# Performance work log

Measured on AMD Instinct MI355X. Metric: run time of the kernel, lower is better.

## Reference

```python
import jax, jax.numpy as jnp
import numpy as np

PATCH = 16      # sqrt(n_patches=256)
ALPHA = 10.0
HEADS, DH = 2, 64


def _fourier(coords, Bm):
    # coords: (HW, 2), Bm: (n_features, 2) -> (HW, 2*n_features)
    proj = 2.0 * jnp.pi * coords @ Bm.T
    return jnp.concatenate([jnp.cos(proj), jnp.sin(proj)], axis=-1)


def _forward(coords_decoding, tokens, B_q, B_l0, B_l1,
             qW, qb, toqW, tokvW, tooW, toob,
             bwW0, bwb0, bwW1, bwb1,
             modW0, modb0, modW1, modb1,
             hvW0, hvb0, outW0, outb0, outW1, outb1):
    B = coords_decoding.shape[0]
    Hh, Ww = coords_decoding.shape[1], coords_decoding.shape[2]
    coords = coords_decoding.reshape(B, -1, coords_decoding.shape[-1])
    grid = coords[0]                      # (HW, 2); coords_modulation is None -> same grid
    HW = grid.shape[0]
    m = tokens.shape[1]

    # patch indices and spatial bias
    row = jnp.clip((grid[:, 0] * PATCH).astype(jnp.int32), 0, PATCH - 1)
    col = jnp.clip((grid[:, 1] * PATCH).astype(jnp.int32), 0, PATCH - 1)
    idx = row * PATCH + col               # (HW,)
    t = idx.astype(jnp.float32) / (PATCH * PATCH)
    pos = (jnp.arange(m, dtype=jnp.float32) + 0.5) / m
    rel = -ALPHA * jnp.abs(t[None, :] - pos[:, None]) ** 2   # (m, HW)
    bias = rel.T                          # (HW, m), broadcast over batch & heads

    # query features (shared across batch)
    xq = jax.nn.relu(_fourier(grid, B_q) @ qW + qb)           # (HW, hd)
    xq_b = jnp.broadcast_to(xq[None], (B, HW, xq.shape[-1]))

    # cross attention with spatial bias
    q = (xq_b @ toqW).reshape(B, HW, HEADS, DH).transpose(0, 2, 1, 3)   # (B,h,HW,Dh)
    kv = tokens @ tokvW                                                  # (B,m,2*inner)
    k, v = jnp.split(kv, 2, axis=-1)
    k = k.reshape(B, m, HEADS, DH).transpose(0, 2, 1, 3)                 # (B,h,m,Dh)
    v = v.reshape(B, m, HEADS, DH).transpose(0, 2, 1, 3)
    sim = jnp.einsum('bhqd,bhkd->bhqk', q, k) * (DH ** -0.5) + bias[None, None]
    attn = jax.nn.softmax(sim, axis=-1)
    o = jnp.einsum('bhqk,bhkd->bhqd', attn, v)
    o = o.transpose(0, 2, 1, 3).reshape(B, HW, HEADS * DH)
    mod = o @ tooW + toob                                                # (B,HW,hd)

    # per-band MLP stack (layer_num = 2)
    def band(Bl, bwW, bwb, mW, mb):
        h = jax.nn.relu(_fourier(grid, Bl) @ bwW + bwb)                  # (HW,hd)
        return jax.nn.relu(h[None] + mod @ mW + mb)                      # (B,HW,hd)

    m0 = band(B_l0, bwW0, bwb0, modW0, modb0)
    m1 = band(B_l1, bwW1, bwb1, modW1, modb1)
    hv0 = m0
    hv1 = jax.nn.relu((m1 + hv0) @ hvW0 + hvb0)
    out = (hv0 @ outW0 + outb0) + (hv1 @ outW1 + outb1)                  # (B,HW,3)
    return out.reshape(B, Hh, Ww, -1)


def setup_inputs() -> dict:
    key = jax.random.key(0)
    ks = jax.random.split(key, 32)
    B, H, W, L = 4, 128, 128, 256
    fd, hd, cd, od = 64, 256, 256, 3
    nf = fd // 2
    inner = HEADS * DH

    def lin(k, i, o):
        return jax.random.normal(k, (i, o), dtype=jnp.float32) / np.sqrt(i).astype(np.float32)

    inp = {}
    inp['coords_decoding'] = jax.random.uniform(ks[0], (B, H, W, 2), dtype=jnp.float32)
    inp['tokens'] = jax.random.normal(ks[1], (B, L, cd), dtype=jnp.float32)
    inp['B_q'] = jax.random.normal(ks[2], (nf, 2), dtype=jnp.float32) / 16.0
    inp['B_l0'] = jax.random.normal(ks[3], (nf, 2), dtype=jnp.float32) / 128.0
    inp['B_l1'] = jax.random.normal(ks[4], (nf, 2), dtype=jnp.float32) / 32.0
    inp['qW'] = lin(ks[5], fd, hd); inp['qb'] = jnp.zeros((hd,), jnp.float32)
    inp['toqW'] = lin(ks[6], hd, inner)
    inp['tokvW'] = lin(ks[7], cd, inner * 2)
    inp['tooW'] = lin(ks[8], inner, hd); inp['toob'] = jnp.zeros((hd,), jnp.float32)
    inp['bwW0'] = lin(ks[9], fd, hd); inp['bwb0'] = jnp.zeros((hd,), jnp.float32)
    inp['bwW1'] = lin(ks[10], fd, hd); inp['bwb1'] = jnp.zeros((hd,), jnp.float32)
    inp['modW0'] = lin(ks[11], hd, hd); inp['modb0'] = jnp.zeros((hd,), jnp.float32)
    inp['modW1'] = lin(ks[12], hd, hd); inp['modb1'] = jnp.zeros((hd,), jnp.float32)
    inp['hvW0'] = lin(ks[13], hd, hd); inp['hvb0'] = jnp.zeros((hd,), jnp.float32)
    inp['outW0'] = lin(ks[14], hd, od); inp['outb0'] = jnp.zeros((od,), jnp.float32)
    inp['outW1'] = lin(ks[15], hd, od); inp['outb1'] = jnp.zeros((od,), jnp.float32)
    return inp


def reference(coords_decoding, tokens, B_q, B_l0, B_l1,
              qW, qb, toqW, tokvW, tooW, toob,
              bwW0, bwb0, bwW1, bwb1,
              modW0, modb0, modW1, modb1,
              hvW0, hvb0, outW0, outb0, outW1, outb1):
    return _forward(coords_decoding, tokens, B_q, B_l0, B_l1,
                    qW, qb, toqW, tokvW, tooW, toob,
                    bwW0, bwb0, bwW1, bwb1,
                    modW0, modb0, modW1, modb1,
                    hvW0, hvb0, outW0, outb0, outW1, outb1)
```

## Files before the change

### kernel.cpp

```cpp
#include <hip/hip_runtime.h>
#include <stdint.h>

constexpr int kHW = 16384;
constexpr int kB  = 4;
constexpr int kM  = 256;

typedef _Float16 half8 __attribute__((ext_vector_type(8)));
typedef __attribute__((ext_vector_type(4))) float f32x4;

__device__ __forceinline__ unsigned short f2h(float f) {
  _Float16 h = (_Float16)f;
  return __builtin_bit_cast(unsigned short, h);
}
__device__ __forceinline__ float h2f(unsigned short u) {
  return (float)__builtin_bit_cast(_Float16, u);
}

__global__ __launch_bounds__(256) void wprep_kernel(
    const float* __restrict__ tooW, const float* __restrict__ modW0,
    const float* __restrict__ modW1, const float* __restrict__ hvW0,
    const float* __restrict__ qW, const float* __restrict__ bwW0,
    const float* __restrict__ bwW1, const float* __restrict__ toqW,
    unsigned short* __restrict__ tooWt, unsigned short* __restrict__ modW0t,
    unsigned short* __restrict__ modW1t, unsigned short* __restrict__ hvW0t,
    unsigned short* __restrict__ qWt, unsigned short* __restrict__ bw0t,
    unsigned short* __restrict__ bw1t, unsigned short* __restrict__ toqWt)
{
  int m = blockIdx.x, tid = threadIdx.x;
  const float* Ws[8] = {tooW, modW0, modW1, hvW0, qW, bwW0, bwW1, toqW};
  unsigned short* Wts[8] = {tooWt, modW0t, modW1t, hvW0t, qWt, bw0t, bw1t, toqWt};
  const int Ks[8] = {128, 256, 256, 256, 64, 64, 64, 256};
  const int Ns[8] = {256, 256, 256, 256, 256, 256, 256, 128};
  const float* W = Ws[m];
  unsigned short* Wt = Wts[m];
  int K = Ks[m], N = Ns[m];
  if (tid < N) {
    for (int kb = 0; kb < K / 8; kb++) {
      unsigned short sv[8];
#pragma unroll
      for (int i = 0; i < 8; i++)
        sv[i] = f2h(W[(kb * 8 + i) * N + tid]);
      *(uint4*)&Wt[tid * K + kb * 8] = *(const uint4*)sv;
    }
  }
}

__global__ __launch_bounds__(256) void kv_kernel(
    const float* __restrict__ tokens, const float* __restrict__ tokvW,
    unsigned short* __restrict__ kn_ws, unsigned short* __restrict__ vt_ws)
{
  __shared__ __align__(16) float tok[256];
  int b = blockIdx.y, j = blockIdx.x, c = threadIdx.x;
  tok[c] = tokens[(b * kM + j) * 256 + c];
  __syncthreads();
  float acc = 0.f;
  for (int i4 = 0; i4 < 64; i4++) {
    float4 t4 = *(const float4*)&tok[i4 * 4];
    acc += t4.x * tokvW[(i4*4+0)*256 + c] + t4.y * tokvW[(i4*4+1)*256 + c]
         + t4.z * tokvW[(i4*4+2)*256 + c] + t4.w * tokvW[(i4*4+3)*256 + c];
  }
  unsigned short hv = f2h(acc);
  if (c < 128) {
    int h = c >> 6, dd = c & 63;
    kn_ws[((size_t)(b*2+h)*256 + j) * 64 + dd] = hv;
  } else {
    int c2 = c - 128;
    int h = c2 >> 6, dd = c2 & 63;
    vt_ws[((size_t)(b*2+h)*64 + dd) * 256 + j] = hv;
  }
}

constexpr int kFPitch = 72;
constexpr int kXPitch = 264;

__global__ __launch_bounds__(256, 2) void feat_kernel(
    const float* __restrict__ coords,
    const float* __restrict__ Bq, const float* __restrict__ Bl0, const float* __restrict__ Bl1,
    const float* __restrict__ qb, const float* __restrict__ bwb0, const float* __restrict__ bwb1,
    const unsigned short* __restrict__ qWt, const unsigned short* __restrict__ bw0t,
    const unsigned short* __restrict__ bw1t, const unsigned short* __restrict__ toqWt,
    float* __restrict__ t_ws, unsigned short* __restrict__ qc_ws,
    unsigned short* __restrict__ h0_hf, unsigned short* __restrict__ h1_hf)
{
  __shared__ __align__(16) unsigned short ff_s[3][32][kFPitch];
  __shared__ __align__(16) unsigned short xq_s[32][kXPitch];
  __shared__ float coords_s[64];

  int tid = threadIdx.x;
  int px0 = blockIdx.x * 32;
  int w = tid >> 6, ln = tid & 63;
  int c = ln & 15, q = ln >> 4;

  if (tid < 64) coords_s[tid] = coords[px0 * 2 + tid];
  __syncthreads();

#pragma unroll
  for (int r = 0; r < 24; r++) {
    int v = r * 256 + tid;
    int mat = v >> 11;
    int p = (v >> 6) & 31;
    int f = v & 63;
    int fr = f & 31;
    const float* Bm = (mat == 0) ? Bq : (mat == 1 ? Bl0 : Bl1);
    float x = coords_s[p * 2 + 0];
    float y = coords_s[p * 2 + 1];
    float proj = 6.283185307179586f * (x * Bm[fr*2+0] + y * Bm[fr*2+1]);
    float s, cc;
    __sincosf(proj, &s, &cc);
    ff_s[mat][p][f] = f2h((f < 32) ? cc : s);
  }
  if (tid < 32) {
    float x = coords_s[tid * 2 + 0];
    float y = coords_s[tid * 2 + 1];
    int row = min(max((int)(x * 16.0f), 0), 15);
    int col = min(max((int)(y * 16.0f), 0), 15);
    t_ws[px0 + tid] = (float)(row * 16 + col) * (1.0f / 256.0f);
  }
  __syncthreads();

  const f32x4 zero4 = {0.f, 0.f, 0.f, 0.f};

  for (int mat = 0; mat < 3; mat++) {
    const unsigned short* Wt = (mat == 0) ? qWt : (mat == 1 ? bw0t : bw1t);
    const float* bias = (mat == 0) ? qb : (mat == 1 ? bwb0 : bwb1);
    f32x4 acc[8];
#pragma unroll
    for (int i = 0; i < 8; i++) acc[i] = zero4;
#pragma unroll
    for (int ks = 0; ks < 2; ks++) {
      int koff = ks * 32 + q * 8;
      half8 bfr[4];
#pragma unroll
      for (int nt = 0; nt < 4; nt++)
        bfr[nt] = *(const half8*)(Wt + (size_t)(w*64 + nt*16 + c) * 64 + koff);
      half8 afr[2];
#pragma unroll
      for (int mt = 0; mt < 2; mt++)
        afr[mt] = *(const half8*)(&ff_s[mat][mt*16 + c][koff]);
#pragma unroll
      for (int mt = 0; mt < 2; mt++)
#pragma unroll
        for (int nt = 0; nt < 4; nt++)
          acc[mt*4+nt] = __builtin_amdgcn_mfma_f32_16x16x32_f16(afr[mt], bfr[nt], acc[mt*4+nt], 0, 0, 0);
    }
    float bv[4];
#pragma unroll
    for (int nt = 0; nt < 4; nt++) bv[nt] = bias[w*64 + nt*16 + c];
#pragma unroll
    for (int mt = 0; mt < 2; mt++)
#pragma unroll
      for (int nt = 0; nt < 4; nt++)
#pragma unroll
        for (int rg = 0; rg < 4; rg++) {
          int row = mt*16 + q*4 + rg, col = w*64 + nt*16 + c;
          unsigned short hv = f2h(fmaxf(acc[mt*4+nt][rg] + bv[nt], 0.f));
          if (mat == 0)      xq_s[row][col] = hv;
          else if (mat == 1) h0_hf[((size_t)(px0 + row)) * 256 + col] = hv;
          else               h1_hf[((size_t)(px0 + row)) * 256 + col] = hv;
        }
  }
  __syncthreads();

  {
    f32x4 acc2[4];
#pragma unroll
    for (int i = 0; i < 4; i++) acc2[i] = zero4;
#pragma unroll
    for (int kt = 0; kt < 8; kt++) {
      int koff = kt * 32 + q * 8;
      half8 bfr[2];
#pragma unroll
      for (int nt = 0; nt < 2; nt++)
        bfr[nt] = *(const half8*)(toqWt + (size_t)(w*32 + nt*16 + c) * 256 + koff);
      half8 afr[2];
#pragma unroll
      for (int mt = 0; mt < 2; mt++)
        afr[mt] = *(const half8*)(&xq_s[mt*16 + c][koff]);
#pragma unroll
      for (int mt = 0; mt < 2; mt++)
#pragma unroll
        for (int nt = 0; nt < 2; nt++)
          acc2[mt*2+nt] = __builtin_amdgcn_mfma_f32_16x16x32_f16(afr[mt], bfr[nt], acc2[mt*2+nt], 0, 0, 0);
    }
#pragma unroll
    for (int mt = 0; mt < 2; mt++)
#pragma unroll
      for (int nt = 0; nt < 2; nt++)
#pragma unroll
        for (int rg = 0; rg < 4; rg++) {
          int row = mt*16 + q*4 + rg, col = w*32 + nt*16 + c;
          qc_ws[((size_t)(px0 + row)) * 128 + col] = f2h(acc2[mt*2+nt][rg]);
        }
  }
}

constexpr int kPPitch = 264;

__global__ __launch_bounds__(256, 2) void attn_kernel(
    const unsigned short* __restrict__ kn_ws,
    const unsigned short* __restrict__ vt_ws,
    const unsigned short* __restrict__ qc_ws,
    const float* __restrict__ t_ws,
    unsigned short* __restrict__ o_hf)
{
  __shared__ __align__(16) unsigned short P_s[32 * kPPitch];
  __shared__ float t_s[32];
  __shared__ float red_max[32][4];
  __shared__ float red_sum[32][4];

  int b = blockIdx.y;
  int px0 = blockIdx.x * 32;
  int tid = threadIdx.x;
  int w = tid >> 6, ln = tid & 63;
  int c = ln & 15, q = ln >> 4;

  if (tid < 32) t_s[tid] = t_ws[px0 + tid];

  const f32x4 zero4 = {0.f, 0.f, 0.f, 0.f};

  for (int h = 0; h < 2; h++) {
    __syncthreads();

    f32x4 acc[8];
#pragma unroll
    for (int i = 0; i < 8; i++) acc[i] = zero4;
    const unsigned short* kbase = kn_ws + (size_t)(b*2+h) * 256 * 64;
#pragma unroll
    for (int ks = 0; ks < 2; ks++) {
      int koff = ks * 32 + q * 8;
      half8 a0 = *(const half8*)(qc_ws + (size_t)(px0 + c) * 128 + h*64 + koff);
      half8 a1 = *(const half8*)(qc_ws + (size_t)(px0 + 16 + c) * 128 + h*64 + koff);
#pragma unroll
      for (int nt = 0; nt < 4; nt++) {
        half8 bf = *(const half8*)(kbase + (size_t)(w*64 + nt*16 + c) * 64 + koff);
        acc[0*4+nt] = __builtin_amdgcn_mfma_f32_16x16x32_f16(a0, bf, acc[0*4+nt], 0, 0, 0);
        acc[1*4+nt] = __builtin_amdgcn_mfma_f32_16x16x32_f16(a1, bf, acc[1*4+nt], 0, 0, 0);
      }
    }

    float lm[2][4];
#pragma unroll
    for (int mt = 0; mt < 2; mt++)
#pragma unroll
      for (int rg = 0; rg < 4; rg++) {
        int row = mt*16 + q*4 + rg;
        float tv = t_s[row];
        float mx = -1e30f;
#pragma unroll
        for (int nt = 0; nt < 4; nt++) {
          int token = w*64 + nt*16 + c;
          float pos = ((float)token + 0.5f) * (1.0f / 256.0f);
          float db = tv - pos;
          float sb = acc[mt*4+nt][rg] * 0.125f - 10.0f * db * db;
          acc[mt*4+nt][rg] = sb;
          mx = fmaxf(mx, sb);
        }
        lm[mt][rg] = mx;
      }
#pragma unroll
    for (int s = 1; s < 16; s <<= 1)
#pragma unroll
      for (int mt = 0; mt < 2; mt++)
#pragma unroll
        for (int rg = 0; rg < 4; rg++)
          lm[mt][rg] = fmaxf(lm[mt][rg], __shfl_xor(lm[mt][rg], s, 64));
    if (c == 0) {
#pragma unroll
      for (int mt = 0; mt < 2; mt++)
#pragma unroll
        for (int rg = 0; rg < 4; rg++)
          red_max[mt*16 + q*4 + rg][w] = lm[mt][rg];
    }
    __syncthreads();

    float ps[2][4];
#pragma unroll
    for (int mt = 0; mt < 2; mt++)
#pragma unroll
      for (int rg = 0; rg < 4; rg++) {
        int row = mt*16 + q*4 + rg;
        float gm = fmaxf(fmaxf(red_max[row][0], red_max[row][1]),
                         fmaxf(red_max[row][2], red_max[row][3]));
        float sum = 0.f;
#pragma unroll
        for (int nt = 0; nt < 4; nt++) {
          float e = __expf(acc[mt*4+nt][rg] - gm);
          sum += e;
          P_s[row * kPPitch + w*64 + nt*16 + c] = f2h(e);
        }
        ps[mt][rg] = sum;
      }
#pragma unroll
    for (int s = 1; s < 16; s <<= 1)
#pragma unroll
      for (int mt = 0; mt < 2; mt++)
#pragma unroll
        for (int rg = 0; rg < 4; rg++)
          ps[mt][rg] += __shfl_xor(ps[mt][rg], s, 64);
    if (c == 0) {
#pragma unroll
      for (int mt = 0; mt < 2; mt++)
#pragma unroll
        for (int rg = 0; rg < 4; rg++)
          red_sum[mt*16 + q*4 + rg][w] = ps[mt][rg];
    }
    __syncthreads();

    f32x4 oacc[2] = {zero4, zero4};
    const unsigned short* vbase = vt_ws + (size_t)(b*2+h) * 64 * 256;
#pragma unroll
    for (int kt = 0; kt < 8; kt++) {
      int koff = kt * 32 + q * 8;
      half8 bf = *(const half8*)(vbase + (size_t)(w*16 + c) * 256 + koff);
      half8 a0 = *(const half8*)(P_s + (0*16 + c) * kPPitch + koff);
      half8 a1 = *(const half8*)(P_s + (1*16 + c) * kPPitch + koff);
      oacc[0] = __builtin_amdgcn_mfma_f32_16x16x32_f16(a0, bf, oacc[0], 0, 0, 0);
      oacc[1] = __builtin_amdgcn_mfma_f32_16x16x32_f16(a1, bf, oacc[1], 0, 0, 0);
    }
#pragma unroll
    for (int mt = 0; mt < 2; mt++)
#pragma unroll
      for (int rg = 0; rg < 4; rg++) {
        int row = mt*16 + q*4 + rg;
        float rinv = 1.0f / (red_sum[row][0] + red_sum[row][1] +
                             red_sum[row][2] + red_sum[row][3]);
        o_hf[((size_t)(b * kHW + px0 + row)) * 128 + h*64 + w*16 + c] =
            f2h(oacc[mt][rg] * rinv);
      }
  }
}

constexpr int kPitch = 264;

template <int KD>
__device__ __forceinline__ void gemm4(
    const unsigned short* abuf, const unsigned short* wt,
    f32x4* acc , int c, int q)
{
#pragma unroll
  for (int ks = 0; ks < KD / 32; ks++) {
    int koff = ks * 32 + q * 8;
    half8 bfr[4];
#pragma unroll
    for (int nt = 0; nt < 4; nt++)
      bfr[nt] = *(const half8*)(wt + (nt * 16 + c) * KD + koff);
    half8 afr[4];
#pragma unroll
    for (int mt = 0; mt < 4; mt++)
      afr[mt] = *(const half8*)(abuf + (mt * 16 + c) * kPitch + koff);
#pragma unroll
    for (int mt = 0; mt < 4; mt++)
#pragma unroll
      for (int nt = 0; nt < 4; nt++)
        acc[mt * 4 + nt] = __builtin_amdgcn_mfma_f32_16x16x32_f16(afr[mt], bfr[nt], acc[mt * 4 + nt], 0, 0, 0);
  }
}

__global__ __launch_bounds__(256, 2) void mlp_kernel(
    const unsigned short* __restrict__ o_hf,
    const unsigned short* __restrict__ h0_hf, const unsigned short* __restrict__ h1_hf,
    const unsigned short* __restrict__ tooWt, const float* __restrict__ toob,
    const unsigned short* __restrict__ modW0t, const float* __restrict__ modb0,
    const unsigned short* __restrict__ modW1t, const float* __restrict__ modb1,
    const unsigned short* __restrict__ hvW0t, const float* __restrict__ hvb0,
    const float* __restrict__ outW0, const float* __restrict__ outb0,
    const float* __restrict__ outW1, const float* __restrict__ outb1,
    float* __restrict__ dout)
{
  __shared__ __align__(16) unsigned short buf0[64 * kPitch];
  __shared__ __align__(16) unsigned short buf1[64 * kPitch];
  __shared__ __align__(16) unsigned short hbuf[16 * kPitch];
  __shared__ __align__(16) float scratch[64 * 3 * 4];

  int tid = threadIdx.x;
  int px0 = blockIdx.x * 16;
  int w = tid >> 6, ln = tid & 63;
  int c = ln & 15, q = ln >> 4;

#pragma unroll
  for (int i = 0; i < 4; i++) {
    int idx = i * 256 + tid;
    int r = idx >> 4, c8 = (idx & 15) * 8;
    int b = r >> 4, px = r & 15;
    uint4 v = *(const uint4*)(o_hf + ((size_t)(b * kHW + px0 + px)) * 128 + c8);
    *(uint4*)&buf0[r * kPitch + c8] = v;
  }
#pragma unroll
  for (int i = 0; i < 2; i++) {
    int idx = i * 256 + tid;
    int p = idx >> 5, c8 = (idx & 31) * 8;
    uint4 v = *(const uint4*)(h0_hf + ((size_t)(px0 + p)) * 256 + c8);
    *(uint4*)&hbuf[p * kPitch + c8] = v;
  }
  __syncthreads();

  f32x4 acc[16];
  const f32x4 zero4 = {0.f, 0.f, 0.f, 0.f};

#pragma unroll
  for (int i = 0; i < 16; i++) acc[i] = zero4;
  gemm4<128>(buf0, tooWt + (size_t)w * 64 * 128, acc, c, q);
  {
    float bias[4];
#pragma unroll
    for (int nt = 0; nt < 4; nt++) bias[nt] = toob[w * 64 + nt * 16 + c];
#pragma unroll
    for (int mt = 0; mt < 4; mt++)
#pragma unroll
      for (int nt = 0; nt < 4; nt++)
#pragma unroll
        for (int rg = 0; rg < 4; rg++) {
          int row = mt * 16 + q * 4 + rg, col = w * 64 + nt * 16 + c;
          buf1[row * kPitch + col] = f2h(acc[mt * 4 + nt][rg] + bias[nt]);
        }
  }
  __syncthreads();

#pragma unroll
  for (int i = 0; i < 16; i++) acc[i] = zero4;
  gemm4<256>(buf1, modW0t + (size_t)w * 64 * 256, acc, c, q);
  {
    float bias[4], hr[4][4];
#pragma unroll
    for (int nt = 0; nt < 4; nt++) {
      int col = w * 64 + nt * 16 + c;
      bias[nt] = modb0[col];
#pragma unroll
      for (int rg = 0; rg < 4; rg++)
        hr[nt][rg] = h2f(hbuf[(q * 4 + rg) * kPitch + col]);
    }
#pragma unroll
    for (int mt = 0; mt < 4; mt++)
#pragma unroll
      for (int nt = 0; nt < 4; nt++)
#pragma unroll
        for (int rg = 0; rg < 4; rg++) {
          int row = mt * 16 + q * 4 + rg, col = w * 64 + nt * 16 + c;
          buf0[row * kPitch + col] =
              f2h(fmaxf(acc[mt * 4 + nt][rg] + bias[nt] + hr[nt][rg], 0.f));
        }
  }
  __syncthreads();

#pragma unroll
  for (int i = 0; i < 2; i++) {
    int idx = i * 256 + tid;
    int p = idx >> 5, c8 = (idx & 31) * 8;
    uint4 v = *(const uint4*)(h1_hf + ((size_t)(px0 + p)) * 256 + c8);
    *(uint4*)&hbuf[p * kPitch + c8] = v;
  }
#pragma unroll
  for (int i = 0; i < 16; i++) acc[i] = zero4;
  gemm4<256>(buf1, modW1t + (size_t)w * 64 * 256, acc, c, q);
  __syncthreads();
  {
    float bias[4], hr[4][4];
#pragma unroll
    for (int nt = 0; nt < 4; nt++) {
      int col = w * 64 + nt * 16 + c;
      bias[nt] = modb1[col];
#pragma unroll
      for (int rg = 0; rg < 4; rg++)
        hr[nt][rg] = h2f(hbuf[(q * 4 + rg) * kPitch + col]);
    }
#pragma unroll
    for (int mt = 0; mt < 4; mt++)
#pragma unroll
      for (int nt = 0; nt < 4; nt++)
#pragma unroll
        for (int rg = 0; rg < 4; rg++) {
          int row = mt * 16 + q * 4 + rg, col = w * 64 + nt * 16 + c;
          float m0v = h2f(buf0[row * kPitch + col]);
          float v = m0v + fmaxf(acc[mt * 4 + nt][rg] + bias[nt] + hr[nt][rg], 0.f);
          buf1[row * kPitch + col] = f2h(v);
        }
  }
  __syncthreads();

#pragma unroll
  for (int i = 0; i < 16; i++) acc[i] = zero4;
  gemm4<256>(buf1, hvW0t + (size_t)w * 64 * 256, acc, c, q);
  {
    float bias[4], w0v[4][3], w1v[4][3];
#pragma unroll
    for (int nt = 0; nt < 4; nt++) {
      int col = w * 64 + nt * 16 + c;
      bias[nt] = hvb0[col];
#pragma unroll
      for (int k = 0; k < 3; k++) {
        w0v[nt][k] = outW0[col * 3 + k];
        w1v[nt][k] = outW1[col * 3 + k];
      }
    }
#pragma unroll
    for (int mt = 0; mt < 4; mt++) {
      float pk[4][3];
#pragma unroll
      for (int rg = 0; rg < 4; rg++)
#pragma unroll
        for (int k = 0; k < 3; k++) pk[rg][k] = 0.f;
#pragma unroll
      for (int nt = 0; nt < 4; nt++) {
        int col = w * 64 + nt * 16 + c;
#pragma unroll
        for (int rg = 0; rg < 4; rg++) {
          int row = mt * 16 + q * 4 + rg;
          float hv1 = fmaxf(acc[mt * 4 + nt][rg] + bias[nt], 0.f);
          float m0v = h2f(buf0[row * kPitch + col]);
#pragma unroll
          for (int k = 0; k < 3; k++)
            pk[rg][k] += m0v * w0v[nt][k] + hv1 * w1v[nt][k];
        }
      }
#pragma unroll
      for (int s = 1; s < 16; s <<= 1)
#pragma unroll
        for (int rg = 0; rg < 4; rg++)
#pragma unroll
          for (int k = 0; k < 3; k++)
            pk[rg][k] += __shfl_xor(pk[rg][k], s, 64);
      if (c == 0) {
#pragma unroll
        for (int rg = 0; rg < 4; rg++) {
          int row = mt * 16 + q * 4 + rg;
#pragma unroll
          for (int k = 0; k < 3; k++)
            scratch[row * 12 + k * 4 + w] = pk[rg][k];
        }
      }
    }
  }
  __syncthreads();

  if (tid < 192) {
    int row = tid / 3, k = tid % 3;
    int b = row >> 4, px = px0 + (row & 15);
    float s = outb0[k] + outb1[k];
#pragma unroll
    for (int ww = 0; ww < 4; ww++) s += scratch[row * 12 + k * 4 + ww];
    dout[((size_t)b * kHW + px) * 3 + k] = s;
  }
}

extern "C" void kernel_launch(void* const* d_in, const int* in_sizes, int n_in,
                              void* d_out, int out_size, void* d_ws, size_t ws_size,
                              hipStream_t stream) {
  const float* coords = (const float*)d_in[0];
  const float* tokens = (const float*)d_in[1];
  const float* Bq     = (const float*)d_in[2];
  const float* Bl0    = (const float*)d_in[3];
  const float* Bl1    = (const float*)d_in[4];
  const float* qW     = (const float*)d_in[5];
  const float* qb     = (const float*)d_in[6];
  const float* toqW   = (const float*)d_in[7];
  const float* tokvW  = (const float*)d_in[8];
  const float* tooW   = (const float*)d_in[9];
  const float* toob   = (const float*)d_in[10];
  const float* bwW0   = (const float*)d_in[11];
  const float* bwb0   = (const float*)d_in[12];
  const float* bwW1   = (const float*)d_in[13];
  const float* bwb1   = (const float*)d_in[14];
  const float* modW0  = (const float*)d_in[15];
  const float* modb0  = (const float*)d_in[16];
  const float* modW1  = (const float*)d_in[17];
  const float* modb1  = (const float*)d_in[18];
  const float* hvW0   = (const float*)d_in[19];
  const float* hvb0   = (const float*)d_in[20];
  const float* outW0  = (const float*)d_in[21];
  const float* outb0  = (const float*)d_in[22];
  const float* outW1  = (const float*)d_in[23];
  const float* outb1  = (const float*)d_in[24];

  char* ws = (char*)d_ws;
  float*          t_ws   = (float*)(ws + 0);
  unsigned short* qc_ws  = (unsigned short*)(ws + 65536);
  unsigned short* h0_hf  = (unsigned short*)(ws + 4259840);
  unsigned short* h1_hf  = (unsigned short*)(ws + 12648448);
  unsigned short* o_hf   = (unsigned short*)(ws + 21037056);
  unsigned short* kn_ws  = (unsigned short*)(ws + 37814272);
  unsigned short* vt_ws  = (unsigned short*)(ws + 38076416);
  unsigned short* tooWt  = (unsigned short*)(ws + 38338560);
  unsigned short* modW0t = (unsigned short*)(ws + 38404096);
  unsigned short* modW1t = (unsigned short*)(ws + 38535168);
  unsigned short* hvW0t  = (unsigned short*)(ws + 38666240);
  unsigned short* qWt    = (unsigned short*)(ws + 38797312);
  unsigned short* bw0t   = (unsigned short*)(ws + 38830080);
  unsigned short* bw1t   = (unsigned short*)(ws + 38862848);
  unsigned short* toqWt  = (unsigned short*)(ws + 38895616);

  wprep_kernel<<<dim3(8), 256, 0, stream>>>(
      tooW, modW0, modW1, hvW0, qW, bwW0, bwW1, toqW,
      tooWt, modW0t, modW1t, hvW0t, qWt, bw0t, bw1t, toqWt);
  feat_kernel<<<dim3(kHW / 32), 256, 0, stream>>>(
      coords, Bq, Bl0, Bl1, qb, bwb0, bwb1,
      qWt, bw0t, bw1t, toqWt,
      t_ws, qc_ws, h0_hf, h1_hf);
  kv_kernel<<<dim3(kM, kB), 256, 0, stream>>>(tokens, tokvW, kn_ws, vt_ws);
  attn_kernel<<<dim3(kHW / 32, kB), 256, 0, stream>>>(kn_ws, vt_ws, qc_ws, t_ws, o_hf);
  mlp_kernel<<<dim3(kHW / 16), 256, 0, stream>>>(
      o_hf, h0_hf, h1_hf, tooWt, toob, modW0t, modb0, modW1t, modb1,
      hvW0t, hvb0, outW0, outb0, outW1, outb1, (float*)d_out);
}
```

Baseline: 258.5 us.

## Prefetch weight fragments and band features into registers in MLP kernel

The MLP GEMM helper now double-prefetches the weight B-fragments two k-steps ahead in a three-slot register ring, so global weight loads overlap the MFMA work. The per-band h0/h1 residual features are loaded directly into registers at kernel start instead of being staged through a shared-memory buffer, which removes that buffer and one barrier. Streaming loads and the final output store use nontemporal hints. The cost is higher register pressure (16 extra half values plus 12 half8 fragments) under a launch bound of two blocks per SIMD, which could cause spills or lower occupancy, and the per-element residual loads are narrower and less coalesced than before.

```diff
diff --git a/kernel.cpp b/kernel.cpp
--- a/kernel.cpp
+++ b/kernel.cpp
@@ -7,6 +7,7 @@
 
 typedef _Float16 half8 __attribute__((ext_vector_type(8)));
 typedef __attribute__((ext_vector_type(4))) float f32x4;
+typedef unsigned int u32x4 __attribute__((ext_vector_type(4)));
 
 __device__ __forceinline__ unsigned short f2h(float f) {
   _Float16 h = (_Float16)f;
@@ -337,22 +338,39 @@
     const unsigned short* abuf, const unsigned short* wt,
     f32x4* acc , int c, int q)
 {
-#pragma unroll
-  for (int ks = 0; ks < KD / 32; ks++) {
+  constexpr int NKS = KD / 32;
+  const unsigned short* wr0 = wt + (0 * 16 + c) * KD + q * 8;
+  const unsigned short* wr1 = wt + (1 * 16 + c) * KD + q * 8;
+  const unsigned short* wr2 = wt + (2 * 16 + c) * KD + q * 8;
+  const unsigned short* wr3 = wt + (3 * 16 + c) * KD + q * 8;
+  half8 bfr[3][4];
+#pragma unroll
+  for (int p = 0; p < 2; p++) {
+    bfr[p][0] = *(const half8*)(wr0 + p * 32);
+    bfr[p][1] = *(const half8*)(wr1 + p * 32);
+    bfr[p][2] = *(const half8*)(wr2 + p * 32);
+    bfr[p][3] = *(const half8*)(wr3 + p * 32);
+  }
+#pragma unroll
+  for (int ks = 0; ks < NKS; ks++) {
+    if (ks + 2 < NKS) {
+      int slot = (ks + 2) % 3, koff2 = (ks + 2) * 32;
+      bfr[slot][0] = *(const half8*)(wr0 + koff2);
+      bfr[slot][1] = *(const half8*)(wr1 + koff2);
+      bfr[slot][2] = *(const half8*)(wr2 + koff2);
+      bfr[slot][3] = *(const half8*)(wr3 + koff2);
+    }
+    half8 afr[4];
     int koff = ks * 32 + q * 8;
-    half8 bfr[4];
-#pragma unroll
-    for (int nt = 0; nt < 4; nt++)
-      bfr[nt] = *(const half8*)(wt + (nt * 16 + c) * KD + koff);
-    half8 afr[4];
 #pragma unroll
     for (int mt = 0; mt < 4; mt++)
       afr[mt] = *(const half8*)(abuf + (mt * 16 + c) * kPitch + koff);
+    int cur = ks % 3;
 #pragma unroll
     for (int mt = 0; mt < 4; mt++)
 #pragma unroll
       for (int nt = 0; nt < 4; nt++)
-        acc[mt * 4 + nt] = __builtin_amdgcn_mfma_f32_16x16x32_f16(afr[mt], bfr[nt], acc[mt * 4 + nt], 0, 0, 0);
+        acc[mt * 4 + nt] = __builtin_amdgcn_mfma_f32_16x16x32_f16(afr[mt], bfr[cur][nt], acc[mt * 4 + nt], 0, 0, 0);
   }
 }
 
@@ -369,33 +387,38 @@
 {
   __shared__ __align__(16) unsigned short buf0[64 * kPitch];
   __shared__ __align__(16) unsigned short buf1[64 * kPitch];
-  __shared__ __align__(16) unsigned short hbuf[16 * kPitch];
-  __shared__ __align__(16) float scratch[64 * 3 * 4];
+  __shared__ float scratch[64 * 12];
 
   int tid = threadIdx.x;
   int px0 = blockIdx.x * 16;
   int w = tid >> 6, ln = tid & 63;
   int c = ln & 15, q = ln >> 4;
 
+  unsigned short h0r[4][4], h1r[4][4];
+#pragma unroll
+  for (int nt = 0; nt < 4; nt++) {
+    int col = w * 64 + nt * 16 + c;
+#pragma unroll
+    for (int rg = 0; rg < 4; rg++) {
+      int px = q * 4 + rg;
+      h0r[nt][rg] = __builtin_nontemporal_load(h0_hf + ((size_t)(px0 + px)) * 256 + col);
+      h1r[nt][rg] = __builtin_nontemporal_load(h1_hf + ((size_t)(px0 + px)) * 256 + col);
+    }
+  }
+
 #pragma unroll
   for (int i = 0; i < 4; i++) {
     int idx = i * 256 + tid;
     int r = idx >> 4, c8 = (idx & 15) * 8;
     int b = r >> 4, px = r & 15;
-    uint4 v = *(const uint4*)(o_hf + ((size_t)(b * kHW + px0 + px)) * 128 + c8);
-    *(uint4*)&buf0[r * kPitch + c8] = v;
-  }
-#pragma unroll
-  for (int i = 0; i < 2; i++) {
-    int idx = i * 256 + tid;
-    int p = idx >> 5, c8 = (idx & 31) * 8;
-    uint4 v = *(const uint4*)(h0_hf + ((size_t)(px0 + p)) * 256 + c8);
-    *(uint4*)&hbuf[p * kPitch + c8] = v;
-  }
-  __syncthreads();
-
+    u32x4 v = __builtin_nontemporal_load(
+        (const u32x4*)(o_hf + ((size_t)(b * kHW + px0 + px)) * 128 + c8));
+    *(u32x4*)&buf0[r * kPitch + c8] = v;
+  }
+  __syncthreads();
+
+  const f32x4 zero4 = {0.f, 0.f, 0.f, 0.f};
   f32x4 acc[16];
-  const f32x4 zero4 = {0.f, 0.f, 0.f, 0.f};
 
 #pragma unroll
   for (int i = 0; i < 16; i++) acc[i] = zero4;
@@ -420,15 +443,9 @@
   for (int i = 0; i < 16; i++) acc[i] = zero4;
   gemm4<256>(buf1, modW0t + (size_t)w * 64 * 256, acc, c, q);
   {
-    float bias[4], hr[4][4];
-#pragma unroll
-    for (int nt = 0; nt < 4; nt++) {
-      int col = w * 64 + nt * 16 + c;
-      bias[nt] = modb0[col];
-#pragma unroll
-      for (int rg = 0; rg < 4; rg++)
-        hr[nt][rg] = h2f(hbuf[(q * 4 + rg) * kPitch + col]);
-    }
+    float bias[4];
+#pragma unroll
+    for (int nt = 0; nt < 4; nt++) bias[nt] = modb0[w * 64 + nt * 16 + c];
 #pragma unroll
     for (int mt = 0; mt < 4; mt++)
 #pragma unroll
@@ -437,32 +454,19 @@
         for (int rg = 0; rg < 4; rg++) {
           int row = mt * 16 + q * 4 + rg, col = w * 64 + nt * 16 + c;
           buf0[row * kPitch + col] =
-              f2h(fmaxf(acc[mt * 4 + nt][rg] + bias[nt] + hr[nt][rg], 0.f));
-        }
-  }
-  __syncthreads();
-
-#pragma unroll
-  for (int i = 0; i < 2; i++) {
-    int idx = i * 256 + tid;
-    int p = idx >> 5, c8 = (idx & 31) * 8;
-    uint4 v = *(const uint4*)(h1_hf + ((size_t)(px0 + p)) * 256 + c8);
-    *(uint4*)&hbuf[p * kPitch + c8] = v;
-  }
+              f2h(fmaxf(acc[mt * 4 + nt][rg] + bias[nt] + h2f(h0r[nt][rg]), 0.f));
+        }
+  }
+  __syncthreads();
+
 #pragma unroll
   for (int i = 0; i < 16; i++) acc[i] = zero4;
   gemm4<256>(buf1, modW1t + (size_t)w * 64 * 256, acc, c, q);
   __syncthreads();
   {
-    float bias[4], hr[4][4];
-#pragma unroll
-    for (int nt = 0; nt < 4; nt++) {
-      int col = w * 64 + nt * 16 + c;
-      bias[nt] = modb1[col];
-#pragma unroll
-      for (int rg = 0; rg < 4; rg++)
-        hr[nt][rg] = h2f(hbuf[(q * 4 + rg) * kPitch + col]);
-    }
+    float bias[4];
+#pragma unroll
+    for (int nt = 0; nt < 4; nt++) bias[nt] = modb1[w * 64 + nt * 16 + c];
 #pragma unroll
     for (int mt = 0; mt < 4; mt++)
 #pragma unroll
@@ -471,7 +475,7 @@
         for (int rg = 0; rg < 4; rg++) {
           int row = mt * 16 + q * 4 + rg, col = w * 64 + nt * 16 + c;
           float m0v = h2f(buf0[row * kPitch + col]);
-          float v = m0v + fmaxf(acc[mt * 4 + nt][rg] + bias[nt] + hr[nt][rg], 0.f);
+          float v = m0v + fmaxf(acc[mt * 4 + nt][rg] + bias[nt] + h2f(h1r[nt][rg]), 0.f);
           buf1[row * kPitch + col] = f2h(v);
         }
   }
@@ -538,7 +542,7 @@
     float s = outb0[k] + outb1[k];
 #pragma unroll
     for (int ww = 0; ww < 4; ww++) s += scratch[row * 12 + k * 4 + ww];
-    dout[((size_t)b * kHW + px) * 3 + k] = s;
+    __builtin_nontemporal_store(s, dout + ((size_t)b * kHW + px) * 3 + k);
   }
 }
 
```

Result: no change. 260.6 us (+0.8%).
